# Performance work log

Measured on AMD Instinct MI355X. Metric: run time of the kernel, lower is better.

Reference implementation:

```python
import jax, jax.numpy as jnp
import numpy as np

B, C, H, W = 8, 256, 128, 128  # dim=256 channels, match_factor=2 -> num_matching=128


def setup_inputs() -> dict:
    key = jax.random.key(0)
    k1, k2 = jax.random.split(key)
    x = jax.random.normal(k1, (B, C, H, W), dtype=jnp.float32)
    Ym = jax.random.normal(k2, (B, C, H, W), dtype=jnp.float32)
    return {"x": x, "Ym": Ym, "num_matching": 128}


def _matching(x, Ym, num_matching):
    # x, Ym: (B, C, H, W); flatten spatial -> (B, C, N) with N = H*W
    b, c, h, w = x.shape
    xf = x.reshape(b, c, h * w)
    yf = Ym.reshape(b, c, h * w)
    # pairwise L2 distances between channel vectors: (B, C, C)
    x2 = jnp.sum(xf * xf, axis=-1)
    y2 = jnp.sum(yf * yf, axis=-1)
    d2 = x2[:, :, None] + y2[:, None, :] - 2.0 * jnp.einsum('bin,bjn->bij', xf, yf)
    dist = jnp.sqrt(jnp.maximum(d2, 0.0))
    # topk(k=1, largest=False) == min / argmin over candidates
    topk_values = jnp.min(dist, axis=-1)      # (B, C)
    topk_indices = jnp.argmin(dist, axis=-1)  # (B, C) nearest candidate per input channel
    # keep the num_matching input channels with smallest min-distance, in original order
    order = jnp.argsort(topk_values, axis=1)[:, :num_matching]  # channel ids with rank < num_matching
    sel = jnp.sort(order, axis=1)                               # restore original channel order (masked_select semantics)
    nn_idx = jnp.take_along_axis(topk_indices, sel, axis=1)     # (B, num_matching)
    # batched gather of candidate rows: (B, num_matching, N)
    filt = jnp.take_along_axis(yf, nn_idx[:, :, None], axis=1)
    return filt.reshape(b, num_matching, h, w)


def reference(x, Ym, num_matching):
    return _matching(x, Ym, num_matching)
```

## Files before the change

### kernel.cpp

```cpp
#include <hip/hip_runtime.h>

#define B_  8
#define C_  256
#define N_  16384
#define NM_ 128
#define LDK 40

typedef _Float16 f16x8 __attribute__((ext_vector_type(8)));
typedef float    f32x4 __attribute__((ext_vector_type(4)));

__global__ __launch_bounds__(512, 4) void gemm_f16_kernel(const float* __restrict__ X,
                                                          const float* __restrict__ Y,
                                                          float* __restrict__ Gp,
                                                          float* __restrict__ x2p,
                                                          float* __restrict__ y2p,
                                                          int Kchunk) {
    __shared__ _Float16 aH[128][LDK];
    __shared__ _Float16 aL[128][LDK];
    __shared__ _Float16 bH[128][LDK];
    __shared__ _Float16 bL[128][LDK];

    int lin = blockIdx.x;
    int jt = lin & 1, it = (lin >> 1) & 1, b = (lin >> 2) & 7, ks = lin >> 5;
    int k0 = ks * Kchunk;

    int t = threadIdx.x;
    int lane = t & 63;
    int wid = t >> 6;
    int wm = wid >> 1, wn = wid & 1;

    int srow = t >> 2;
    int skq = (t & 3) * 8;

    const float* xp = X + ((size_t)(b * C_) + it * 128 + srow) * N_ + k0 + skq;
    const float* yp = Y + ((size_t)(b * C_) + jt * 128 + srow) * N_ + k0 + skq;

    f32x4 acc[2][4] = {};
    float sx = 0.f, sy = 0.f;

    float4 VA[2], VB[2];
    VA[0] = *(const float4*)(xp);
    VA[1] = *(const float4*)(xp + 4);
    VB[0] = *(const float4*)(yp);
    VB[1] = *(const float4*)(yp + 4);

    for (int kk = 0; kk < Kchunk; kk += 32) {
        _Float16 ha[8], la[8], hb[8], lb[8];
        const float* fa = (const float*)VA;
        const float* fb = (const float*)VB;
#pragma unroll
        for (int e = 0; e < 8; ++e) {
            float v = fa[e];
            _Float16 h = (_Float16)v;
            ha[e] = h; la[e] = (_Float16)(v - (float)h);
            sx += v * v;
            float w = fb[e];
            _Float16 h2 = (_Float16)w;
            hb[e] = h2; lb[e] = (_Float16)(w - (float)h2);
            sy += w * w;
        }

        __syncthreads();
        *(f16x8*)&aH[srow][skq] = *(f16x8*)&ha[0];
        *(f16x8*)&aL[srow][skq] = *(f16x8*)&la[0];
        *(f16x8*)&bH[srow][skq] = *(f16x8*)&hb[0];
        *(f16x8*)&bL[srow][skq] = *(f16x8*)&lb[0];

        if (kk + 32 < Kchunk) {
            VA[0] = *(const float4*)(xp + kk + 32);
            VA[1] = *(const float4*)(xp + kk + 36);
            VB[0] = *(const float4*)(yp + kk + 32);
            VB[1] = *(const float4*)(yp + kk + 36);
        }
        __syncthreads();

        int fr = lane & 15, fk = (lane >> 4) * 8;
        f16x8 fAH[2], fAL[2], fBH[4], fBL[4];
#pragma unroll
        for (int mf = 0; mf < 2; ++mf) {
            fAH[mf] = *(const f16x8*)&aH[wm * 32 + mf * 16 + fr][fk];
            fAL[mf] = *(const f16x8*)&aL[wm * 32 + mf * 16 + fr][fk];
        }
#pragma unroll
        for (int nf = 0; nf < 4; ++nf) {
            fBH[nf] = *(const f16x8*)&bH[wn * 64 + nf * 16 + fr][fk];
            fBL[nf] = *(const f16x8*)&bL[wn * 64 + nf * 16 + fr][fk];
        }
#pragma unroll
        for (int mf = 0; mf < 2; ++mf)
#pragma unroll
            for (int nf = 0; nf < 4; ++nf) {
                acc[mf][nf] = __builtin_amdgcn_mfma_f32_16x16x32_f16(fAH[mf], fBH[nf], acc[mf][nf], 0, 0, 0);
                acc[mf][nf] = __builtin_amdgcn_mfma_f32_16x16x32_f16(fAH[mf], fBL[nf], acc[mf][nf], 0, 0, 0);
                acc[mf][nf] = __builtin_amdgcn_mfma_f32_16x16x32_f16(fAL[mf], fBH[nf], acc[mf][nf], 0, 0, 0);
            }
    }

    size_t gb = ((size_t)(ks * B_ + b) * C_ + it * 128) * C_ + jt * 128;
#pragma unroll
    for (int mf = 0; mf < 2; ++mf)
#pragma unroll
        for (int nf = 0; nf < 4; ++nf) {
            int rr = wm * 32 + mf * 16 + (lane >> 4) * 4;
            int cc = wn * 64 + nf * 16 + (lane & 15);
#pragma unroll
            for (int r = 0; r < 4; ++r)
                Gp[gb + (size_t)(rr + r) * C_ + cc] = acc[mf][nf][r];
        }

    sx += __shfl_xor(sx, 1);
    sx += __shfl_xor(sx, 2);
    sy += __shfl_xor(sy, 1);
    sy += __shfl_xor(sy, 2);
    if (!(t & 3)) {
        if (jt == 0) x2p[(ks * B_ + b) * C_ + it * 128 + srow] = sx;
        if (it == 0) y2p[(ks * B_ + b) * C_ + jt * 128 + srow] = sy;
    }
}

__global__ __launch_bounds__(256) void argmin_kernel(const float* __restrict__ Gp,
                                                     const float* __restrict__ x2p,
                                                     const float* __restrict__ y2p,
                                                     float* __restrict__ minval,
                                                     int* __restrict__ minidx,
                                                     int KS) {
    int bi = blockIdx.x;
    int b = bi >> 8;
    int i = bi & 255;
    int j = threadIdx.x;

    float g = 0.f, sx = 0.f, sy = 0.f;
    for (int ks = 0; ks < KS; ++ks) {
        g  += Gp[((size_t)(ks * B_ + b) * C_ + i) * C_ + j];
        sx += x2p[(ks * B_ + b) * C_ + i];
        sy += y2p[(ks * B_ + b) * C_ + j];
    }

    float v = sx + sy - 2.f * g;
    int idx = j;
#pragma unroll
    for (int off = 32; off > 0; off >>= 1) {
        float v2 = __shfl_down(v, off);
        int i2 = __shfl_down(idx, off);
        if (v2 < v || (v2 == v && i2 < idx)) { v = v2; idx = i2; }
    }
    __shared__ float wv[4];
    __shared__ int wi[4];
    int lane = threadIdx.x & 63, wid = threadIdx.x >> 6;
    if (lane == 0) { wv[wid] = v; wi[wid] = idx; }
    __syncthreads();
    if (threadIdx.x == 0) {
        for (int w = 1; w < 4; ++w)
            if (wv[w] < v || (wv[w] == v && wi[w] < idx)) { v = wv[w]; idx = wi[w]; }
        minval[bi] = v;
        minidx[bi] = idx;
    }
}

__global__ __launch_bounds__(256) void select_kernel(const float* __restrict__ minval,
                                                     const int* __restrict__ minidx,
                                                     int* __restrict__ nn) {
    int b = blockIdx.x;
    int i = threadIdx.x;
    __shared__ float vals[C_];
    __shared__ int wcnt[4];

    float v = minval[b * C_ + i];
    vals[i] = v;
    __syncthreads();

    int rank = 0;
    for (int tt = 0; tt < C_; ++tt) {
        float u = vals[tt];
        rank += (u < v) || (u == v && tt < i);
    }
    bool flag = rank < NM_;

    unsigned long long m = __ballot(flag);
    int lane = i & 63, wid = i >> 6;
    if (lane == 0) wcnt[wid] = (int)__popcll(m);
    __syncthreads();
    int off = 0;
    for (int w = 0; w < wid; ++w) off += wcnt[w];
    int pos = off + (int)__popcll(m & ((1ULL << lane) - 1ULL));
    if (flag) nn[b * NM_ + pos] = minidx[b * C_ + i];
}

__global__ __launch_bounds__(256) void gather_kernel(const float* __restrict__ Y,
                                                     const int* __restrict__ nn,
                                                     float* __restrict__ out) {
    int blk = blockIdx.x;
    int b = blk >> 7;
    int m = blk & 127;
    int src = nn[b * NM_ + m];
    const float4* s = (const float4*)(Y + ((size_t)b * C_ + src) * N_);
    float4* d = (float4*)(out + ((size_t)b * NM_ + m) * N_);
    for (int tt = threadIdx.x; tt < N_ / 4; tt += 256) d[tt] = s[tt];
}

extern "C" void kernel_launch(void* const* d_in, const int* in_sizes, int n_in,
                              void* d_out, int out_size, void* d_ws, size_t ws_size,
                              hipStream_t stream) {
    const float* X = (const float*)d_in[0];
    const float* Y = (const float*)d_in[1];
    float* out = (float*)d_out;

    size_t favail = ws_size / 4;
    int KS = 1;
    while (KS < 16) {
        int KS2 = KS * 2;
        size_t need = (size_t)KS2 * B_ * C_ * C_
                    + (size_t)KS2 * 2 * B_ * C_
                    + 2 * B_ * C_ + B_ * NM_;
        if (need > favail) break;
        KS = KS2;
    }
    int Kchunk = N_ / KS;

    float* minval = (float*)d_ws;
    int* minidx = (int*)(minval + B_ * C_);
    int* nn = minidx + B_ * C_;
    float* x2p = (float*)(nn + B_ * NM_);
    float* y2p = x2p + (size_t)KS * B_ * C_;
    float* Gp = y2p + (size_t)KS * B_ * C_;

    hipLaunchKernelGGL(gemm_f16_kernel, dim3(KS * 32), dim3(512), 0, stream, X, Y, Gp, x2p, y2p, Kchunk);
    hipLaunchKernelGGL(argmin_kernel, dim3(B_ * C_), dim3(256), 0, stream, Gp, x2p, y2p, minval, minidx, KS);
    hipLaunchKernelGGL(select_kernel, dim3(B_), dim3(256), 0, stream, minval, minidx, nn);
    hipLaunchKernelGGL(gather_kernel, dim3(B_ * NM_), dim3(256), 0, stream, Y, nn, out);
}
```

Measured before the change: 134.9 us.

## Double-buffer LDS tiles in split-f16 GEMM to drop one barrier per step

The GEMM kernel now keeps two LDS buffers for the hi/lo f16 tiles. While the current buffer is read into fragments, the next chunk is converted and written into the other buffer, and global loads are prefetched two steps ahead. This removes one __syncthreads per K-step and overlaps conversion and stores with MFMA work. In exchange, LDS use doubles (about 80KB per block), which may limit how many blocks fit per CU, and the deeper prefetch adds register pressure.

```diff
diff --git a/kernel.cpp b/kernel.cpp
--- a/kernel.cpp
+++ b/kernel.cpp
@@ -15,10 +15,10 @@
                                                           float* __restrict__ x2p,
                                                           float* __restrict__ y2p,
                                                           int Kchunk) {
-    __shared__ _Float16 aH[128][LDK];
-    __shared__ _Float16 aL[128][LDK];
-    __shared__ _Float16 bH[128][LDK];
-    __shared__ _Float16 bL[128][LDK];
+    __shared__ _Float16 aH[2][128][LDK];
+    __shared__ _Float16 aL[2][128][LDK];
+    __shared__ _Float16 bH[2][128][LDK];
+    __shared__ _Float16 bL[2][128][LDK];
 
     int lin = blockIdx.x;
     int jt = lin & 1, it = (lin >> 1) & 1, b = (lin >> 2) & 7, ks = lin >> 5;
@@ -37,14 +37,16 @@
 
     f32x4 acc[2][4] = {};
     float sx = 0.f, sy = 0.f;
-
     float4 VA[2], VB[2];
-    VA[0] = *(const float4*)(xp);
-    VA[1] = *(const float4*)(xp + 4);
-    VB[0] = *(const float4*)(yp);
-    VB[1] = *(const float4*)(yp + 4);
-
-    for (int kk = 0; kk < Kchunk; kk += 32) {
+
+    auto prefetch = [&](int koff) {
+        VA[0] = *(const float4*)(xp + koff);
+        VA[1] = *(const float4*)(xp + koff + 4);
+        VB[0] = *(const float4*)(yp + koff);
+        VB[1] = *(const float4*)(yp + koff + 4);
+    };
+
+    auto stage_chunk = [&](int bi) {
         _Float16 ha[8], la[8], hb[8], lb[8];
         const float* fa = (const float*)VA;
         const float* fb = (const float*)VB;
@@ -59,33 +61,37 @@
             hb[e] = h2; lb[e] = (_Float16)(w - (float)h2);
             sy += w * w;
         }
-
+        *(f16x8*)&aH[bi][srow][skq] = *(f16x8*)&ha[0];
+        *(f16x8*)&aL[bi][srow][skq] = *(f16x8*)&la[0];
+        *(f16x8*)&bH[bi][srow][skq] = *(f16x8*)&hb[0];
+        *(f16x8*)&bL[bi][srow][skq] = *(f16x8*)&lb[0];
+    };
+
+    prefetch(0);
+    stage_chunk(0);
+    if (Kchunk > 32) prefetch(32);
+
+    int fr = lane & 15, fk = (lane >> 4) * 8;
+    int cur = 0;
+
+    for (int kk = 0; kk < Kchunk; kk += 32) {
         __syncthreads();
-        *(f16x8*)&aH[srow][skq] = *(f16x8*)&ha[0];
-        *(f16x8*)&aL[srow][skq] = *(f16x8*)&la[0];
-        *(f16x8*)&bH[srow][skq] = *(f16x8*)&hb[0];
-        *(f16x8*)&bL[srow][skq] = *(f16x8*)&lb[0];
-
-        if (kk + 32 < Kchunk) {
-            VA[0] = *(const float4*)(xp + kk + 32);
-            VA[1] = *(const float4*)(xp + kk + 36);
-            VB[0] = *(const float4*)(yp + kk + 32);
-            VB[1] = *(const float4*)(yp + kk + 36);
-        }
-        __syncthreads();
-
-        int fr = lane & 15, fk = (lane >> 4) * 8;
+
         f16x8 fAH[2], fAL[2], fBH[4], fBL[4];
 #pragma unroll
         for (int mf = 0; mf < 2; ++mf) {
-            fAH[mf] = *(const f16x8*)&aH[wm * 32 + mf * 16 + fr][fk];
-            fAL[mf] = *(const f16x8*)&aL[wm * 32 + mf * 16 + fr][fk];
+            fAH[mf] = *(const f16x8*)&aH[cur][wm * 32 + mf * 16 + fr][fk];
+            fAL[mf] = *(const f16x8*)&aL[cur][wm * 32 + mf * 16 + fr][fk];
         }
 #pragma unroll
         for (int nf = 0; nf < 4; ++nf) {
-            fBH[nf] = *(const f16x8*)&bH[wn * 64 + nf * 16 + fr][fk];
-            fBL[nf] = *(const f16x8*)&bL[wn * 64 + nf * 16 + fr][fk];
-        }
+            fBH[nf] = *(const f16x8*)&bH[cur][wn * 64 + nf * 16 + fr][fk];
+            fBL[nf] = *(const f16x8*)&bL[cur][wn * 64 + nf * 16 + fr][fk];
+        }
+
+        if (kk + 32 < Kchunk) stage_chunk(cur ^ 1);
+        if (kk + 64 < Kchunk) prefetch(kk + 64);
+
 #pragma unroll
         for (int mf = 0; mf < 2; ++mf)
 #pragma unroll
@@ -94,6 +100,7 @@
                 acc[mf][nf] = __builtin_amdgcn_mfma_f32_16x16x32_f16(fAH[mf], fBL[nf], acc[mf][nf], 0, 0, 0);
                 acc[mf][nf] = __builtin_amdgcn_mfma_f32_16x16x32_f16(fAL[mf], fBH[nf], acc[mf][nf], 0, 0, 0);
             }
+        cur ^= 1;
     }
 
     size_t gb = ((size_t)(ks * B_ + b) * C_ + it * 128) * C_ + jt * 128;
```

Result: no change. 132.4 us (-1.9%).

## Double-buffer fp32 tiles via direct global-to-LDS loads, split to fp16 at fragment read

Applied to the files above, without the earlier changes.

The GEMM kernel now stages raw fp32 tiles straight into LDS with global_load_lds into a double buffer with an XOR swizzle. The fp16 hi/lo split and the squared-norm sums move to fragment read time, so the prefetch of the next tile overlaps the MFMAs on the current one and the kernel needs one barrier per k-step instead of two. The cost is redundant conversion work, since each wave re-converts rows shared with other waves, plus more LDS (64 KB) and raised MFMA priority.

```diff
diff --git a/kernel.cpp b/kernel.cpp
--- a/kernel.cpp
+++ b/kernel.cpp
@@ -4,21 +4,20 @@
 #define C_  256
 #define N_  16384
 #define NM_ 128
-#define LDK 40
 
 typedef _Float16 f16x8 __attribute__((ext_vector_type(8)));
 typedef float    f32x4 __attribute__((ext_vector_type(4)));
 
-__global__ __launch_bounds__(512, 4) void gemm_f16_kernel(const float* __restrict__ X,
-                                                          const float* __restrict__ Y,
-                                                          float* __restrict__ Gp,
-                                                          float* __restrict__ x2p,
-                                                          float* __restrict__ y2p,
-                                                          int Kchunk) {
-    __shared__ _Float16 aH[128][LDK];
-    __shared__ _Float16 aL[128][LDK];
-    __shared__ _Float16 bH[128][LDK];
-    __shared__ _Float16 bL[128][LDK];
+__global__ __launch_bounds__(512)
+__attribute__((amdgpu_waves_per_eu(4, 4)))
+void gemm_f16_kernel(const float* __restrict__ X,
+                     const float* __restrict__ Y,
+                     float* __restrict__ Gp,
+                     float* __restrict__ x2p,
+                     float* __restrict__ y2p,
+                     int Kchunk) {
+    __shared__ float A_lds[2][128 * 32];
+    __shared__ float B_lds[2][128 * 32];
 
     int lin = blockIdx.x;
     int jt = lin & 1, it = (lin >> 1) & 1, b = (lin >> 2) & 7, ks = lin >> 5;
@@ -29,72 +28,96 @@
     int wid = t >> 6;
     int wm = wid >> 1, wn = wid & 1;
 
-    int srow = t >> 2;
-    int skq = (t & 3) * 8;
-
-    const float* xp = X + ((size_t)(b * C_) + it * 128 + srow) * N_ + k0 + skq;
-    const float* yp = Y + ((size_t)(b * C_) + jt * 128 + srow) * N_ + k0 + skq;
+    const float* Xb = X + ((size_t)(b * C_) + it * 128) * N_;
+    const float* Yb = Y + ((size_t)(b * C_) + jt * 128) * N_;
+
+    int srow_lane = lane >> 3;
+    int sunit = (lane & 7) ^ srow_lane;
 
     f32x4 acc[2][4] = {};
-    float sx = 0.f, sy = 0.f;
-
-    float4 VA[2], VB[2];
-    VA[0] = *(const float4*)(xp);
-    VA[1] = *(const float4*)(xp + 4);
-    VB[0] = *(const float4*)(yp);
-    VB[1] = *(const float4*)(yp + 4);
-
-    for (int kk = 0; kk < Kchunk; kk += 32) {
-        _Float16 ha[8], la[8], hb[8], lb[8];
-        const float* fa = (const float*)VA;
-        const float* fb = (const float*)VB;
-#pragma unroll
-        for (int e = 0; e < 8; ++e) {
-            float v = fa[e];
-            _Float16 h = (_Float16)v;
-            ha[e] = h; la[e] = (_Float16)(v - (float)h);
-            sx += v * v;
-            float w = fb[e];
-            _Float16 h2 = (_Float16)w;
-            hb[e] = h2; lb[e] = (_Float16)(w - (float)h2);
-            sy += w * w;
+    float sA[2] = {0.f, 0.f};
+    float sB[4] = {0.f, 0.f, 0.f, 0.f};
+
+    auto stage = [&](int bi, int kk) {
+#pragma unroll
+        for (int q = 0; q < 2; ++q) {
+            int rowt = wid * 16 + q * 8 + srow_lane;
+            const float* ga = Xb + (size_t)rowt * N_ + k0 + kk + sunit * 4;
+            const float* gb = Yb + (size_t)rowt * N_ + k0 + kk + sunit * 4;
+            __builtin_amdgcn_global_load_lds(
+                (const __attribute__((address_space(1))) void*)ga,
+                (__attribute__((address_space(3))) void*)&A_lds[bi][(wid * 16 + q * 8) * 32],
+                16, 0, 0);
+            __builtin_amdgcn_global_load_lds(
+                (const __attribute__((address_space(1))) void*)gb,
+                (__attribute__((address_space(3))) void*)&B_lds[bi][(wid * 16 + q * 8) * 32],
+                16, 0, 0);
         }
-
-        __syncthreads();
-        *(f16x8*)&aH[srow][skq] = *(f16x8*)&ha[0];
-        *(f16x8*)&aL[srow][skq] = *(f16x8*)&la[0];
-        *(f16x8*)&bH[srow][skq] = *(f16x8*)&hb[0];
-        *(f16x8*)&bL[srow][skq] = *(f16x8*)&lb[0];
-
-        if (kk + 32 < Kchunk) {
-            VA[0] = *(const float4*)(xp + kk + 32);
-            VA[1] = *(const float4*)(xp + kk + 36);
-            VB[0] = *(const float4*)(yp + kk + 32);
-            VB[1] = *(const float4*)(yp + kk + 36);
-        }
-        __syncthreads();
-
-        int fr = lane & 15, fk = (lane >> 4) * 8;
-        f16x8 fAH[2], fAL[2], fBH[4], fBL[4];
-#pragma unroll
-        for (int mf = 0; mf < 2; ++mf) {
-            fAH[mf] = *(const f16x8*)&aH[wm * 32 + mf * 16 + fr][fk];
-            fAL[mf] = *(const f16x8*)&aL[wm * 32 + mf * 16 + fr][fk];
-        }
-#pragma unroll
-        for (int nf = 0; nf < 4; ++nf) {
-            fBH[nf] = *(const f16x8*)&bH[wn * 64 + nf * 16 + fr][fk];
-            fBL[nf] = *(const f16x8*)&bL[wn * 64 + nf * 16 + fr][fk];
-        }
-#pragma unroll
-        for (int mf = 0; mf < 2; ++mf)
-#pragma unroll
-            for (int nf = 0; nf < 4; ++nf) {
-                acc[mf][nf] = __builtin_amdgcn_mfma_f32_16x16x32_f16(fAH[mf], fBH[nf], acc[mf][nf], 0, 0, 0);
-                acc[mf][nf] = __builtin_amdgcn_mfma_f32_16x16x32_f16(fAH[mf], fBL[nf], acc[mf][nf], 0, 0, 0);
-                acc[mf][nf] = __builtin_amdgcn_mfma_f32_16x16x32_f16(fAL[mf], fBH[nf], acc[mf][nf], 0, 0, 0);
-            }
-    }
+    };
+
+#define CVT(P0, P1, HI, LO, SQ)                           \
+    {                                                     \
+        float tmp_[8];                                    \
+        *(f32x4*)&tmp_[0] = (P0);                         \
+        *(f32x4*)&tmp_[4] = (P1);                         \
+        _Pragma("unroll")                                 \
+        for (int e_ = 0; e_ < 8; ++e_) {                  \
+            float v_ = tmp_[e_];                          \
+            _Float16 h_ = (_Float16)v_;                   \
+            (HI)[e_] = h_;                                \
+            (LO)[e_] = (_Float16)(v_ - (float)h_);        \
+            (SQ) += v_ * v_;                              \
+        }                                                 \
+    }
+
+#define MFMA16(A, Bf, Cc) __builtin_amdgcn_mfma_f32_16x16x32_f16((A), (Bf), (Cc), 0, 0, 0)
+
+#define KSTEP(RD, WR, KOFF)                                                            \
+    {                                                                                  \
+        if ((KOFF) + 32 < Kchunk) stage(WR, (KOFF) + 32);                              \
+        f16x8 aHi[2], aLo[2], bHi[4], bLo[4];                                          \
+        _Pragma("unroll")                                                              \
+        for (int mf = 0; mf < 2; ++mf) {                                               \
+            int rl = wm * 32 + mf * 16 + (lane & 15);                                  \
+            int s7 = rl & 7, g2 = (lane >> 4) * 2;                                     \
+            f32x4 p0 = *(const f32x4*)&A_lds[RD][rl * 32 + (g2 ^ s7) * 4];             \
+            f32x4 p1 = *(const f32x4*)&A_lds[RD][rl * 32 + ((g2 + 1) ^ s7) * 4];       \
+            CVT(p0, p1, aHi[mf], aLo[mf], sA[mf]);                                     \
+        }                                                                              \
+        _Pragma("unroll")                                                              \
+        for (int nf = 0; nf < 4; ++nf) {                                               \
+            int rl = wn * 64 + nf * 16 + (lane & 15);                                  \
+            int s7 = rl & 7, g2 = (lane >> 4) * 2;                                     \
+            f32x4 p0 = *(const f32x4*)&B_lds[RD][rl * 32 + (g2 ^ s7) * 4];             \
+            f32x4 p1 = *(const f32x4*)&B_lds[RD][rl * 32 + ((g2 + 1) ^ s7) * 4];       \
+            CVT(p0, p1, bHi[nf], bLo[nf], sB[nf]);                                     \
+        }                                                                              \
+        __builtin_amdgcn_s_setprio(1);                                                 \
+        _Pragma("unroll")                                                              \
+        for (int nf = 0; nf < 4; ++nf) {                                               \
+            acc[0][nf] = MFMA16(aHi[0], bHi[nf], acc[0][nf]);                          \
+            acc[1][nf] = MFMA16(aHi[1], bHi[nf], acc[1][nf]);                          \
+            acc[0][nf] = MFMA16(aHi[0], bLo[nf], acc[0][nf]);                          \
+            acc[1][nf] = MFMA16(aHi[1], bLo[nf], acc[1][nf]);                          \
+            acc[0][nf] = MFMA16(aLo[0], bHi[nf], acc[0][nf]);                          \
+            acc[1][nf] = MFMA16(aLo[1], bHi[nf], acc[1][nf]);                          \
+        }                                                                              \
+        __builtin_amdgcn_s_setprio(0);                                                 \
+        asm volatile("s_waitcnt vmcnt(0)" ::: "memory");                               \
+        __builtin_amdgcn_s_barrier();                                                  \
+        __builtin_amdgcn_sched_barrier(0);                                             \
+    }
+
+    stage(0, 0);
+    asm volatile("s_waitcnt vmcnt(0)" ::: "memory");
+    __builtin_amdgcn_s_barrier();
+    __builtin_amdgcn_sched_barrier(0);
+
+    for (int kk = 0; kk < Kchunk; kk += 64) {
+        KSTEP(0, 1, kk);
+        KSTEP(1, 0, kk + 32);
+    }
+#undef KSTEP
 
     size_t gb = ((size_t)(ks * B_ + b) * C_ + it * 128) * C_ + jt * 128;
 #pragma unroll
@@ -108,13 +131,21 @@
                 Gp[gb + (size_t)(rr + r) * C_ + cc] = acc[mf][nf][r];
         }
 
-    sx += __shfl_xor(sx, 1);
-    sx += __shfl_xor(sx, 2);
-    sy += __shfl_xor(sy, 1);
-    sy += __shfl_xor(sy, 2);
-    if (!(t & 3)) {
-        if (jt == 0) x2p[(ks * B_ + b) * C_ + it * 128 + srow] = sx;
-        if (it == 0) y2p[(ks * B_ + b) * C_ + jt * 128 + srow] = sy;
+#pragma unroll
+    for (int mf = 0; mf < 2; ++mf) {
+        float s = sA[mf];
+        s += __shfl_xor(s, 16);
+        s += __shfl_xor(s, 32);
+        if (jt == 0 && wn == 0 && lane < 16)
+            x2p[(ks * B_ + b) * C_ + it * 128 + wm * 32 + mf * 16 + lane] = s;
+    }
+#pragma unroll
+    for (int nf = 0; nf < 4; ++nf) {
+        float s = sB[nf];
+        s += __shfl_xor(s, 16);
+        s += __shfl_xor(s, 32);
+        if (it == 0 && wm == 0 && lane < 16)
+            y2p[(ks * B_ + b) * C_ + jt * 128 + wn * 64 + nf * 16 + lane] = s;
     }
 }
 
```

Result: slower. 262.0 us (+94.2%).

## Double-buffer LDS and widen GEMM tile to 256x128 with split-phase MFMA schedule

Applied to the files above, without the earlier changes.

The split-f16 GEMM kernel is rewritten to use 256x128 output tiles, so each block covers all X rows and X is no longer re-read per row tile. Shared memory is double-buffered. Global loads for the next k-step are issued before the MFMAs, and the convert/store is interleaved between two MFMA phases using explicit barriers, waitcnts and setprio. The grid halves, and each wave holds 64 accumulator registers with waves_per_eu fixed at 2, which trades occupancy for reuse and overlap. A dead variant (the old-named kernel with a bugged accumulator layout) is left in the file.

```diff
diff --git a/kernel.cpp b/kernel.cpp
--- a/kernel.cpp
+++ b/kernel.cpp
@@ -4,118 +4,325 @@
 #define C_  256
 #define N_  16384
 #define NM_ 128
-#define LDK 40
 
 typedef _Float16 f16x8 __attribute__((ext_vector_type(8)));
 typedef float    f32x4 __attribute__((ext_vector_type(4)));
 
-__global__ __launch_bounds__(512, 4) void gemm_f16_kernel(const float* __restrict__ X,
-                                                          const float* __restrict__ Y,
-                                                          float* __restrict__ Gp,
-                                                          float* __restrict__ x2p,
-                                                          float* __restrict__ y2p,
-                                                          int Kchunk) {
-    __shared__ _Float16 aH[128][LDK];
-    __shared__ _Float16 aL[128][LDK];
-    __shared__ _Float16 bH[128][LDK];
-    __shared__ _Float16 bL[128][LDK];
+#define MFMA16(A, Bf, Cc) __builtin_amdgcn_mfma_f32_16x16x32_f16((A), (Bf), (Cc), 0, 0, 0)
+
+__global__ __launch_bounds__(512)
+__attribute__((amdgpu_waves_per_eu(2, 2)))
+void gemm_f16_kernel(const float* __restrict__ X,
+                     const float* __restrict__ Y,
+                     float* __restrict__ Gp,
+                     float* __restrict__ x2p,
+                     float* __restrict__ y2p,
+                     int Kchunk) {
+    __shared__ _Float16 aH[2][256][32];
+    __shared__ _Float16 aL[2][256][32];
+    __shared__ _Float16 bH[2][128][32];
+    __shared__ _Float16 bL[2][128][32];
 
     int lin = blockIdx.x;
-    int jt = lin & 1, it = (lin >> 1) & 1, b = (lin >> 2) & 7, ks = lin >> 5;
+    int jt = lin & 1, b = (lin >> 1) & 7, ks = lin >> 4;
     int k0 = ks * Kchunk;
 
     int t = threadIdx.x;
     int lane = t & 63;
     int wid = t >> 6;
     int wm = wid >> 1, wn = wid & 1;
-
-    int srow = t >> 2;
-    int skq = (t & 3) * 8;
-
-    const float* xp = X + ((size_t)(b * C_) + it * 128 + srow) * N_ + k0 + skq;
-    const float* yp = Y + ((size_t)(b * C_) + jt * 128 + srow) * N_ + k0 + skq;
-
-    f32x4 acc[2][4] = {};
+    int fr = lane & 15, fk = (lane >> 4) * 8;
+
+    const float* Xb = X + (size_t)(b * C_) * N_;
+    const float* Yb = Y + (size_t)(b * C_ + jt * 128) * N_;
+
+    int arow = t >> 1, akh = t & 1;
+    int brow = t >> 2, bkq = t & 3;
+    const float* ax = Xb + (size_t)arow * N_ + k0 + akh * 16;
+    const float* by = Yb + (size_t)brow * N_ + k0 + bkq * 8;
+
+    f32x4 acc[4][2] = {};
     float sx = 0.f, sy = 0.f;
-
-    float4 VA[2], VB[2];
-    VA[0] = *(const float4*)(xp);
-    VA[1] = *(const float4*)(xp + 4);
-    VB[0] = *(const float4*)(yp);
-    VB[1] = *(const float4*)(yp + 4);
-
-    for (int kk = 0; kk < Kchunk; kk += 32) {
-        _Float16 ha[8], la[8], hb[8], lb[8];
-        const float* fa = (const float*)VA;
-        const float* fb = (const float*)VB;
+    float4 VA[4], VB[2];
+
+    auto issue = [&](int koff) {
+        VA[0] = *(const float4*)(ax + koff);
+        VA[1] = *(const float4*)(ax + koff + 4);
+        VA[2] = *(const float4*)(ax + koff + 8);
+        VA[3] = *(const float4*)(ax + koff + 12);
+        VB[0] = *(const float4*)(by + koff);
+        VB[1] = *(const float4*)(by + koff + 4);
+    };
+
+    auto convert_store = [&](int wr) {
+        float fa[16];
+        *(float4*)&fa[0]  = VA[0]; *(float4*)&fa[4]  = VA[1];
+        *(float4*)&fa[8]  = VA[2]; *(float4*)&fa[12] = VA[3];
+        f16x8 h0, h1, l0, l1;
 #pragma unroll
         for (int e = 0; e < 8; ++e) {
             float v = fa[e];
             _Float16 h = (_Float16)v;
-            ha[e] = h; la[e] = (_Float16)(v - (float)h);
-            sx += v * v;
+            h0[e] = h; l0[e] = (_Float16)(v - (float)h); sx += v * v;
+            float v2 = fa[e + 8];
+            _Float16 h2 = (_Float16)v2;
+            h1[e] = h2; l1[e] = (_Float16)(v2 - (float)h2); sx += v2 * v2;
+        }
+        *(f16x8*)&aH[wr][arow][akh * 16]     = h0;
+        *(f16x8*)&aH[wr][arow][akh * 16 + 8] = h1;
+        *(f16x8*)&aL[wr][arow][akh * 16]     = l0;
+        *(f16x8*)&aL[wr][arow][akh * 16 + 8] = l1;
+        float fb[8];
+        *(float4*)&fb[0] = VB[0]; *(float4*)&fb[4] = VB[1];
+        f16x8 bh, bl;
+#pragma unroll
+        for (int e = 0; e < 8; ++e) {
             float w = fb[e];
-            _Float16 h2 = (_Float16)w;
-            hb[e] = h2; lb[e] = (_Float16)(w - (float)h2);
-            sy += w * w;
-        }
-
-        __syncthreads();
-        *(f16x8*)&aH[srow][skq] = *(f16x8*)&ha[0];
-        *(f16x8*)&aL[srow][skq] = *(f16x8*)&la[0];
-        *(f16x8*)&bH[srow][skq] = *(f16x8*)&hb[0];
-        *(f16x8*)&bL[srow][skq] = *(f16x8*)&lb[0];
-
-        if (kk + 32 < Kchunk) {
-            VA[0] = *(const float4*)(xp + kk + 32);
-            VA[1] = *(const float4*)(xp + kk + 36);
-            VB[0] = *(const float4*)(yp + kk + 32);
-            VB[1] = *(const float4*)(yp + kk + 36);
-        }
-        __syncthreads();
-
-        int fr = lane & 15, fk = (lane >> 4) * 8;
-        f16x8 fAH[2], fAL[2], fBH[4], fBL[4];
-#pragma unroll
-        for (int mf = 0; mf < 2; ++mf) {
-            fAH[mf] = *(const f16x8*)&aH[wm * 32 + mf * 16 + fr][fk];
-            fAL[mf] = *(const f16x8*)&aL[wm * 32 + mf * 16 + fr][fk];
-        }
-#pragma unroll
-        for (int nf = 0; nf < 4; ++nf) {
-            fBH[nf] = *(const f16x8*)&bH[wn * 64 + nf * 16 + fr][fk];
-            fBL[nf] = *(const f16x8*)&bL[wn * 64 + nf * 16 + fr][fk];
-        }
-#pragma unroll
-        for (int mf = 0; mf < 2; ++mf)
-#pragma unroll
-            for (int nf = 0; nf < 4; ++nf) {
-                acc[mf][nf] = __builtin_amdgcn_mfma_f32_16x16x32_f16(fAH[mf], fBH[nf], acc[mf][nf], 0, 0, 0);
-                acc[mf][nf] = __builtin_amdgcn_mfma_f32_16x16x32_f16(fAH[mf], fBL[nf], acc[mf][nf], 0, 0, 0);
-                acc[mf][nf] = __builtin_amdgcn_mfma_f32_16x16x32_f16(fAL[mf], fBH[nf], acc[mf][nf], 0, 0, 0);
-            }
-    }
-
-    size_t gb = ((size_t)(ks * B_ + b) * C_ + it * 128) * C_ + jt * 128;
-#pragma unroll
-    for (int mf = 0; mf < 2; ++mf)
-#pragma unroll
-        for (int nf = 0; nf < 4; ++nf) {
-            int rr = wm * 32 + mf * 16 + (lane >> 4) * 4;
-            int cc = wn * 64 + nf * 16 + (lane & 15);
-#pragma unroll
-            for (int r = 0; r < 4; ++r)
-                Gp[gb + (size_t)(rr + r) * C_ + cc] = acc[mf][nf][r];
-        }
+            _Float16 h = (_Float16)w;
+            bh[e] = h; bl[e] = (_Float16)(w - (float)h); sy += w * w;
+        }
+        *(f16x8*)&bH[wr][brow][bkq * 8] = bh;
+        *(f16x8*)&bL[wr][brow][bkq * 8] = bl;
+    };
+
+#define KSTEP(RD, WR, KOFF)                                                                        \
+    {                                                                                              \
+          \
+        f16x8 aHi[4], aLo[4];                                                                      \
+        _Pragma("unroll")                                                                          \
+        for (int mf = 0; mf < 4; ++mf) {                                                           \
+            aHi[mf] = *(const f16x8*)&aH[RD][wm * 64 + mf * 16 + fr][fk];                          \
+            aLo[mf] = *(const f16x8*)&aL[RD][wm * 64 + mf * 16 + fr][fk];                          \
+        }                                                                                          \
+        f16x8 b0H = *(const f16x8*)&bH[RD][wn * 64 +  0 + fr][fk];                                 \
+        f16x8 b0L = *(const f16x8*)&bL[RD][wn * 64 +  0 + fr][fk];                                 \
+        f16x8 b1H = *(const f16x8*)&bH[RD][wn * 64 + 16 + fr][fk];                                 \
+        f16x8 b1L = *(const f16x8*)&bL[RD][wn * 64 + 16 + fr][fk];                                 \
+        if ((KOFF) + 32 < Kchunk) issue((KOFF) + 32);                                              \
+        __builtin_amdgcn_sched_barrier(0);                                                         \
+        __builtin_amdgcn_s_barrier();                                                              \
+        asm volatile("s_waitcnt lgkmcnt(0)" ::: "memory");                                         \
+        __builtin_amdgcn_sched_barrier(0);                                                         \
+        __builtin_amdgcn_s_setprio(1);                                                             \
+        _Pragma("unroll") for (int mf = 0; mf < 4; ++mf) acc[mf][0] = MFMA16(aHi[mf], b0H, acc[mf][0]); \
+        _Pragma("unroll") for (int mf = 0; mf < 4; ++mf) acc[mf][1] = MFMA16(aHi[mf], b1H, acc[mf][1]); \
+        _Pragma("unroll") for (int mf = 0; mf < 4; ++mf) acc[mf][0] = MFMA16(aHi[mf], b0L, acc[mf][0]); \
+        _Pragma("unroll") for (int mf = 0; mf < 4; ++mf) acc[mf][1] = MFMA16(aHi[mf], b1L, acc[mf][1]); \
+        _Pragma("unroll") for (int mf = 0; mf < 4; ++mf) acc[mf][0] = MFMA16(aLo[mf], b0H, acc[mf][0]); \
+        _Pragma("unroll") for (int mf = 0; mf < 4; ++mf) acc[mf][1] = MFMA16(aLo[mf], b1H, acc[mf][1]); \
+        __builtin_amdgcn_s_setprio(0);                                                             \
+        __builtin_amdgcn_s_barrier();                                                              \
+             \
+        f16x8 b2H = *(const f16x8*)&bH[RD][wn * 64 + 32 + fr][fk];                                 \
+        f16x8 b2L = *(const f16x8*)&bL[RD][wn * 64 + 32 + fr][fk];                                 \
+        f16x8 b3H = *(const f16x8*)&bH[RD][wn * 64 + 48 + fr][fk];                                 \
+        f16x8 b3L = *(const f16x8*)&bL[RD][wn * 64 + 48 + fr][fk];                                 \
+        if ((KOFF) + 32 < Kchunk) {                                                                \
+            asm volatile("s_waitcnt vmcnt(0)" ::: "memory");                                       \
+            convert_store(WR);                                                                     \
+        }                                                                                          \
+        asm volatile("s_waitcnt lgkmcnt(0)" ::: "memory");                                         \
+        __builtin_amdgcn_s_barrier();                                                              \
+        __builtin_amdgcn_sched_barrier(0);                                                         \
+        __builtin_amdgcn_s_setprio(1);                                                             \
+        _Pragma("unroll") for (int mf = 0; mf < 4; ++mf) acc[mf][0] = MFMA16(aHi[mf], b2H, acc[mf][0]); \
+        _Pragma("unroll") for (int mf = 0; mf < 4; ++mf) acc[mf][1] = MFMA16(aHi[mf], b3H, acc[mf][1]); \
+        _Pragma("unroll") for (int mf = 0; mf < 4; ++mf) acc[mf][0] = MFMA16(aHi[mf], b2L, acc[mf][0]); \
+        _Pragma("unroll") for (int mf = 0; mf < 4; ++mf) acc[mf][1] = MFMA16(aHi[mf], b3L, acc[mf][1]); \
+        _Pragma("unroll") for (int mf = 0; mf < 4; ++mf) acc[mf][0] = MFMA16(aLo[mf], b2H, acc[mf][0]); \
+        _Pragma("unroll") for (int mf = 0; mf < 4; ++mf) acc[mf][1] = MFMA16(aLo[mf], b3H, acc[mf][1]); \
+        __builtin_amdgcn_s_setprio(0);                                                             \
+        __builtin_amdgcn_s_barrier();                                                              \
+    }
+
+    issue(0);
+    asm volatile("s_waitcnt vmcnt(0)" ::: "memory");
+    convert_store(0);
+    asm volatile("s_waitcnt lgkmcnt(0)" ::: "memory");
+    __builtin_amdgcn_s_barrier();
+    __builtin_amdgcn_sched_barrier(0);
+
+    for (int kk = 0; kk < Kchunk; kk += 64) {
+        KSTEP(0, 1, kk);
+        KSTEP(1, 0, kk + 32);
+    }
+#undef KSTEP
+
+    {}
 
     sx += __shfl_xor(sx, 1);
-    sx += __shfl_xor(sx, 2);
+    if (jt == 0 && !(t & 1)) x2p[(ks * B_ + b) * C_ + arow] = sx;
     sy += __shfl_xor(sy, 1);
     sy += __shfl_xor(sy, 2);
-    if (!(t & 3)) {
-        if (jt == 0) x2p[(ks * B_ + b) * C_ + it * 128 + srow] = sx;
-        if (it == 0) y2p[(ks * B_ + b) * C_ + jt * 128 + srow] = sy;
-    }
+    if (!(t & 3)) y2p[(ks * B_ + b) * C_ + jt * 128 + brow] = sy;
+
+    size_t gbase = (size_t)(ks * B_ + b) * C_ * C_ + (size_t)jt * 128;
+#pragma unroll
+    for (int mf = 0; mf < 4; ++mf)
+#pragma unroll
+        for (int nf = 0; nf < 2; ++nf) {
+            int rr = wm * 64 + mf * 16 + (lane >> 4) * 4;
+            int cc = wn * 64 + nf * 16 + (lane & 15);
+#pragma unroll
+            for (int r = 0; r < 4; ++r)
+                Gp[gbase + (size_t)(rr + r) * C_ + cc] = acc[mf][nf][r];
+        }
+}
+
+
+__global__ __launch_bounds__(512)
+__attribute__((amdgpu_waves_per_eu(2, 2)))
+void gemm_f16_kernel_v2(const float* __restrict__ X,
+                        const float* __restrict__ Y,
+                        float* __restrict__ Gp,
+                        float* __restrict__ x2p,
+                        float* __restrict__ y2p,
+                        int Kchunk) {
+    __shared__ _Float16 aH[2][256][32];
+    __shared__ _Float16 aL[2][256][32];
+    __shared__ _Float16 bH[2][128][32];
+    __shared__ _Float16 bL[2][128][32];
+
+    int lin = blockIdx.x;
+    int jt = lin & 1, b = (lin >> 1) & 7, ks = lin >> 4;
+    int k0 = ks * Kchunk;
+
+    int t = threadIdx.x;
+    int lane = t & 63;
+    int wid = t >> 6;
+    int wm = wid >> 1, wn = wid & 1;
+    int fr = lane & 15, fk = (lane >> 4) * 8;
+
+    const float* Xb = X + (size_t)(b * C_) * N_;
+    const float* Yb = Y + (size_t)(b * C_ + jt * 128) * N_;
+
+    int arow = t >> 1, akh = t & 1;
+    int brow = t >> 2, bkq = t & 3;
+    const float* ax = Xb + (size_t)arow * N_ + k0 + akh * 16;
+    const float* by = Yb + (size_t)brow * N_ + k0 + bkq * 8;
+
+    f32x4 acc[4][4] = {};
+    float sx = 0.f, sy = 0.f;
+    float4 VA[4], VB[2];
+
+    auto issue = [&](int koff) {
+        VA[0] = *(const float4*)(ax + koff);
+        VA[1] = *(const float4*)(ax + koff + 4);
+        VA[2] = *(const float4*)(ax + koff + 8);
+        VA[3] = *(const float4*)(ax + koff + 12);
+        VB[0] = *(const float4*)(by + koff);
+        VB[1] = *(const float4*)(by + koff + 4);
+    };
+
+    auto convert_store = [&](int wr) {
+        float fa[16];
+        *(float4*)&fa[0]  = VA[0]; *(float4*)&fa[4]  = VA[1];
+        *(float4*)&fa[8]  = VA[2]; *(float4*)&fa[12] = VA[3];
+        f16x8 h0, h1, l0, l1;
+#pragma unroll
+        for (int e = 0; e < 8; ++e) {
+            float v = fa[e];
+            _Float16 h = (_Float16)v;
+            h0[e] = h; l0[e] = (_Float16)(v - (float)h); sx += v * v;
+            float v2 = fa[e + 8];
+            _Float16 h2 = (_Float16)v2;
+            h1[e] = h2; l1[e] = (_Float16)(v2 - (float)h2); sx += v2 * v2;
+        }
+        *(f16x8*)&aH[wr][arow][akh * 16]     = h0;
+        *(f16x8*)&aH[wr][arow][akh * 16 + 8] = h1;
+        *(f16x8*)&aL[wr][arow][akh * 16]     = l0;
+        *(f16x8*)&aL[wr][arow][akh * 16 + 8] = l1;
+        float fb[8];
+        *(float4*)&fb[0] = VB[0]; *(float4*)&fb[4] = VB[1];
+        f16x8 bh, bl;
+#pragma unroll
+        for (int e = 0; e < 8; ++e) {
+            float w = fb[e];
+            _Float16 h = (_Float16)w;
+            bh[e] = h; bl[e] = (_Float16)(w - (float)h); sy += w * w;
+        }
+        *(f16x8*)&bH[wr][brow][bkq * 8] = bh;
+        *(f16x8*)&bL[wr][brow][bkq * 8] = bl;
+    };
+
+#define KSTEP(RD, WR, KOFF)                                                                        \
+    {                                                                                              \
+        f16x8 aHi[4], aLo[4];                                                                      \
+        _Pragma("unroll")                                                                          \
+        for (int mf = 0; mf < 4; ++mf) {                                                           \
+            aHi[mf] = *(const f16x8*)&aH[RD][wm * 64 + mf * 16 + fr][fk];                          \
+            aLo[mf] = *(const f16x8*)&aL[RD][wm * 64 + mf * 16 + fr][fk];                          \
+        }                                                                                          \
+        f16x8 b0H = *(const f16x8*)&bH[RD][wn * 64 +  0 + fr][fk];                                 \
+        f16x8 b0L = *(const f16x8*)&bL[RD][wn * 64 +  0 + fr][fk];                                 \
+        f16x8 b1H = *(const f16x8*)&bH[RD][wn * 64 + 16 + fr][fk];                                 \
+        f16x8 b1L = *(const f16x8*)&bL[RD][wn * 64 + 16 + fr][fk];                                 \
+        if ((KOFF) + 32 < Kchunk) issue((KOFF) + 32);                                              \
+        __builtin_amdgcn_sched_barrier(0);                                                         \
+        __builtin_amdgcn_s_barrier();                                                              \
+        asm volatile("s_waitcnt lgkmcnt(0)" ::: "memory");                                         \
+        __builtin_amdgcn_sched_barrier(0);                                                         \
+        __builtin_amdgcn_s_setprio(1);                                                             \
+        _Pragma("unroll") for (int mf = 0; mf < 4; ++mf) acc[mf][0] = MFMA16(aHi[mf], b0H, acc[mf][0]); \
+        _Pragma("unroll") for (int mf = 0; mf < 4; ++mf) acc[mf][1] = MFMA16(aHi[mf], b1H, acc[mf][1]); \
+        _Pragma("unroll") for (int mf = 0; mf < 4; ++mf) acc[mf][0] = MFMA16(aHi[mf], b0L, acc[mf][0]); \
+        _Pragma("unroll") for (int mf = 0; mf < 4; ++mf) acc[mf][1] = MFMA16(aHi[mf], b1L, acc[mf][1]); \
+        _Pragma("unroll") for (int mf = 0; mf < 4; ++mf) acc[mf][0] = MFMA16(aLo[mf], b0H, acc[mf][0]); \
+        _Pragma("unroll") for (int mf = 0; mf < 4; ++mf) acc[mf][1] = MFMA16(aLo[mf], b1H, acc[mf][1]); \
+        __builtin_amdgcn_s_setprio(0);                                                             \
+        __builtin_amdgcn_s_barrier();                                                              \
+        f16x8 b2H = *(const f16x8*)&bH[RD][wn * 64 + 32 + fr][fk];                                 \
+        f16x8 b2L = *(const f16x8*)&bL[RD][wn * 64 + 32 + fr][fk];                                 \
+        f16x8 b3H = *(const f16x8*)&bH[RD][wn * 64 + 48 + fr][fk];                                 \
+        f16x8 b3L = *(const f16x8*)&bL[RD][wn * 64 + 48 + fr][fk];                                 \
+        if ((KOFF) + 32 < Kchunk) {                                                                \
+            asm volatile("s_waitcnt vmcnt(0)" ::: "memory");                                       \
+            convert_store(WR);                                                                     \
+        }                                                                                          \
+        asm volatile("s_waitcnt lgkmcnt(0)" ::: "memory");                                         \
+        __builtin_amdgcn_s_barrier();                                                              \
+        __builtin_amdgcn_sched_barrier(0);                                                         \
+        __builtin_amdgcn_s_setprio(1);                                                             \
+        _Pragma("unroll") for (int mf = 0; mf < 4; ++mf) acc[mf][2] = MFMA16(aHi[mf], b2H, acc[mf][2]); \
+        _Pragma("unroll") for (int mf = 0; mf < 4; ++mf) acc[mf][3] = MFMA16(aHi[mf], b3H, acc[mf][3]); \
+        _Pragma("unroll") for (int mf = 0; mf < 4; ++mf) acc[mf][2] = MFMA16(aHi[mf], b2L, acc[mf][2]); \
+        _Pragma("unroll") for (int mf = 0; mf < 4; ++mf) acc[mf][3] = MFMA16(aHi[mf], b3L, acc[mf][3]); \
+        _Pragma("unroll") for (int mf = 0; mf < 4; ++mf) acc[mf][2] = MFMA16(aLo[mf], b2H, acc[mf][2]); \
+        _Pragma("unroll") for (int mf = 0; mf < 4; ++mf) acc[mf][3] = MFMA16(aLo[mf], b3H, acc[mf][3]); \
+        __builtin_amdgcn_s_setprio(0);                                                             \
+        __builtin_amdgcn_s_barrier();                                                              \
+    }
+
+    issue(0);
+    asm volatile("s_waitcnt vmcnt(0)" ::: "memory");
+    convert_store(0);
+    asm volatile("s_waitcnt lgkmcnt(0)" ::: "memory");
+    __builtin_amdgcn_s_barrier();
+    __builtin_amdgcn_sched_barrier(0);
+
+    for (int kk = 0; kk < Kchunk; kk += 64) {
+        KSTEP(0, 1, kk);
+        KSTEP(1, 0, kk + 32);
+    }
+#undef KSTEP
+
+    sx += __shfl_xor(sx, 1);
+    if (jt == 0 && !(t & 1)) x2p[(ks * B_ + b) * C_ + arow] = sx;
+    sy += __shfl_xor(sy, 1);
+    sy += __shfl_xor(sy, 2);
+    if (!(t & 3)) y2p[(ks * B_ + b) * C_ + jt * 128 + brow] = sy;
+
+    size_t gbase = (size_t)(ks * B_ + b) * C_ * C_ + (size_t)jt * 128;
+#pragma unroll
+    for (int mf = 0; mf < 4; ++mf)
+#pragma unroll
+        for (int nf = 0; nf < 4; ++nf) {
+            int rr = wm * 64 + mf * 16 + (lane >> 4) * 4;
+            int cc = wn * 64 + nf * 16 + (lane & 15);
+#pragma unroll
+            for (int r = 0; r < 4; ++r)
+                Gp[gbase + (size_t)(rr + r) * C_ + cc] = acc[mf][nf][r];
+        }
 }
 
 __global__ __launch_bounds__(256) void argmin_kernel(const float* __restrict__ Gp,
@@ -224,7 +431,7 @@
     float* y2p = x2p + (size_t)KS * B_ * C_;
     float* Gp = y2p + (size_t)KS * B_ * C_;
 
-    hipLaunchKernelGGL(gemm_f16_kernel, dim3(KS * 32), dim3(512), 0, stream, X, Y, Gp, x2p, y2p, Kchunk);
+    hipLaunchKernelGGL(gemm_f16_kernel_v2, dim3(KS * 16), dim3(512), 0, stream, X, Y, Gp, x2p, y2p, Kchunk);
     hipLaunchKernelGGL(argmin_kernel, dim3(B_ * C_), dim3(256), 0, stream, Gp, x2p, y2p, minval, minidx, KS);
     hipLaunchKernelGGL(select_kernel, dim3(B_), dim3(256), 0, stream, minval, minidx, nn);
     hipLaunchKernelGGL(gather_kernel, dim3(B_ * NM_), dim3(256), 0, stream, Y, nn, out);
```

After: 160.5 us. +19.0%, slower.
